# Optimization experiments

Hardware: AMD Instinct MI355X
Metric: run time of the kernel (lower is better)

The kernel has to match this reference:

```python
import jax, jax.numpy as jnp
import numpy as np
from math import comb

N_DERIV = 4          # num_derivatives
ODE_DIM = 512        # ode_dimension
K = ODE_DIM * (N_DERIV + 1)


def _build_system(n, d):
    # system_matrices_1d: A_1d = flip(pascal), Q_1d = flip(hilbert), chol(Q_1d)
    x = np.arange(n + 1)
    B = np.array([[comb(i, j) for j in range(n + 1)] for i in range(n + 1)], dtype=np.float64)
    A1 = B[::-1, ::-1]                                  # flip both axes
    Hil = 1.0 / (x[:, None] + x[None, :] + 1.0)
    Q1 = Hil[::-1, ::-1]
    L1 = np.linalg.cholesky(Q1)
    a = np.kron(np.eye(d), A1)
    q = np.kron(np.eye(d), L1)
    return jnp.asarray(a, jnp.float32), jnp.asarray(q, jnp.float32)


def _qr_r(x):
    # sqrtm_to_cholesky: upper-triangular factor from reduced QR
    return jnp.linalg.qr(x)[1]


def setup_inputs() -> dict:
    key = jax.random.key(0)
    k1, k2, k3, k4, k5 = jax.random.split(key, 5)
    a, q_sqrtm_lower = _build_system(N_DERIV, ODE_DIM)
    m0 = jax.random.normal(k1, (K,), dtype=jnp.float32)
    l0 = jnp.tril(jax.random.normal(k2, (K, K), dtype=jnp.float32) * 0.05)
    H = jax.random.normal(k3, (ODE_DIM, K), dtype=jnp.float32) * 0.1
    bias = jax.random.normal(k4, (ODE_DIM,), dtype=jnp.float32)
    dt = jax.random.uniform(k5, (1,), dtype=jnp.float32, minval=0.05, maxval=0.15)
    return {"m0": m0, "l0": l0, "H": H, "bias": bias, "dt": dt,
            "a": a, "q_sqrtm_lower": q_sqrtm_lower}


def reference(m0, l0, H, bias, dt, a, q_sqrtm_lower):
    d = H.shape[0]
    k = m0.shape[0]
    n1 = k // d                       # num_derivatives + 1
    # --- assemble_preconditioner ---
    powers = jnp.arange(n1 - 1, -1, -1, dtype=m0.dtype)
    scales = jnp.exp(jax.lax.lgamma(powers + 1.0))
    pw = powers + 0.5
    adt = jnp.abs(dt[0])
    p = jnp.tile(adt ** pw / scales, d)          # (k,)
    p_inv = jnp.tile(adt ** (-pw) * scales, d)   # (k,)
    # --- extrapolate_mean ---
    m0_p = p_inv * m0
    m_ext_p = a @ m0_p
    m_ext = p * m_ext_p
    # EK-style linearized observation residual
    m_obs = H @ m_ext - bias                     # (d,)
    # --- estimate_error ---
    l_obs_ns_e = H @ (p_inv[:, None] * q_sqrtm_lower)            # (d,k)
    l_obs_raw = _qr_r(l_obs_ns_e.T).T                            # lower (d,d)
    res_white = jax.scipy.linalg.solve_triangular(l_obs_raw.T, m_obs, lower=False)
    diffusion = jnp.sqrt(jnp.dot(res_white, res_white) / res_white.size)
    error = diffusion * jnp.sqrt(jnp.einsum('nj,nj->n', l_obs_raw, l_obs_raw))
    # --- complete_extrapolation (sum_of_sqrtm_factors) ---
    R1 = (a @ (p_inv[:, None] * l0)).T           # (k,k)
    R2 = (diffusion * q_sqrtm_lower).T           # (k,k)
    l_ext_p = _qr_r(jnp.vstack([R1, R2])).T      # lower (k,k)
    l_ext = p[:, None] * l_ext_p
    # --- final_correction ---
    l_obs_ns = H @ l_ext                         # (d,k)
    l_obs = _qr_r(l_obs_ns.T).T                  # lower (d,d)
    crosscov = l_ext @ l_obs_ns.T                # (k,d)
    gain = jax.scipy.linalg.cho_solve((l_obs, True), crosscov.T).T  # (k,d)
    m_cor = m_ext - gain @ m_obs
    l_cor = l_ext - gain @ l_obs_ns
    u = jnp.reshape(m_cor, (-1, d), order='F')[0]  # derivative-0 block
    return m_cor, l_cor, u, error, diffusion
```

## Files before the change

### kernel.cpp

```cpp
#include <hip/hip_runtime.h>
#include <math.h>

#define KDIM 2560
#define DDIM 512
#define NB 64

#define QM 2560
#define QM2 1024
#define QN 512
#define PW 32
#define UW 3
#define QACT 544

#define OUT_LCOR 2560
#define OUT_U    6556160
#define OUT_ERR  6556672
#define OUT_DIFF 6557184


__global__ void k_setup(const float* dt, double* scal){
  if (threadIdx.x==0 && blockIdx.x==0){
    double adt = fabs((double)dt[0]);
    const double scales[5] = {24.0,6.0,2.0,1.0,1.0};
    for (int i=0;i<5;i++){
      double pw = (double)(4-i)+0.5;
      scal[i]   = pow(adt, pw)/scales[i];
      scal[5+i] = pow(adt,-pw)*scales[i];
    }
  }
}

__global__ __launch_bounds__(256) void k_mext_mobs(const float* a, const float* m0, const float* H,
                                                   const float* bias, const double* scal,
                                                   double* mext, double* mobs){
  __shared__ double me[KDIM];
  __shared__ double red[256];
  double pp[5], pv[5];
  #pragma unroll
  for (int i=0;i<5;i++){ pp[i]=scal[i]; pv[i]=scal[5+i]; }
  int tid=threadIdx.x;
  for (int r=tid; r<KDIM; r+=256){
    int j=r/5, i=r%5;
    const float* arow = a + (size_t)r*KDIM + 5*j;
    const float* m0b  = m0 + 5*j;
    double acc=0;
    #pragma unroll
    for (int l=0;l<5;l++) acc += (double)arow[l]*pv[l]*(double)m0b[l];
    me[r] = pp[i]*acc;
  }
  __syncthreads();
  if (blockIdx.x==0) for (int r=tid;r<KDIM;r+=256) mext[r]=me[r];
  int b = blockIdx.x;
  const float* Hr = H + (size_t)b*KDIM;
  double acc=0;
  for (int c=tid;c<KDIM;c+=256) acc += (double)Hr[c]*me[c];
  red[tid]=acc; __syncthreads();
  for (int s=128;s>0;s>>=1){ if (tid<s) red[tid]+=red[tid+s]; __syncthreads(); }
  if (tid==0) mobs[b] = red[0] - (double)bias[b];
}

__global__ void k_A2(const float* H, const float* q, const double* scal,
                     double* Atop, double* Abot){
  int idx = blockIdx.x*blockDim.x+threadIdx.x;
  if (idx >= QN*QM) return;
  double pv[5];
  #pragma unroll
  for (int t=0;t<5;t++) pv[t]=scal[5+t];
  int j = idx / QM;
  int i = idx % QM;
  int bi = i/5;
  double acc=0;
  #pragma unroll
  for (int t=0;t<5;t++)
    acc += (double)H[(size_t)j*QM + 5*bi+t]*pv[t]*(double)q[(size_t)(5*bi+t)*QM + i];
  if (i < 512) Atop[(size_t)j*QM2 + i] = acc;
  else         Abot[(size_t)j*2048 + (i-512)] = acc;
}

__global__ void k_copyB(const double* Gbot, double* AQ){
  int idx = blockIdx.x*blockDim.x+threadIdx.x;
  if (idx >= 512*512) return;
  int c = idx/512, rr = idx%512;
  AQ[(size_t)c*QM2 + 512 + rr] = (rr<=c) ? Gbot[(size_t)c*512 + rr] : 0.0;
}

__global__ __launch_bounds__(576) void qr_panel(double* A, double* vhead, int col0, double* Tbuf){
  __shared__ double redw[9][PW];
  __shared__ double rednorm[9];
  __shared__ double sh[3];
  __shared__ double wsh[PW];
  __shared__ double alphas[PW], betas[PW];
  __shared__ double VtVs[PW][PW];
  __shared__ double Tsh[PW][PW];
  int tid=threadIdx.x, wid=tid>>6, lane=tid&63;
  int m = QM2 - col0; if (m > QACT) m = QACT;
  bool on = tid < m;
  double x[PW];
  #pragma unroll
  for (int j=0;j<PW;j++)
    x[j] = on ? A[(size_t)(col0+j)*QM2 + col0 + tid] : 0.0;
  for (int j=0;j<PW;j++){
    double v0 = (tid>=j && on)? x[j] : 0.0;
    double ps = v0*v0;
    #pragma unroll
    for (int o=32;o>0;o>>=1) ps += __shfl_down(ps,o);
    if (lane==0) rednorm[wid]=ps;
    if (tid==j) sh[0]=x[j];
    __syncthreads();
    if (tid==0){
      double s0=0;
      for (int t=0;t<9;t++) s0+=rednorm[t];
      double x1=sh[0];
      double nrm=sqrt(s0);
      double alpha=(x1>=0.0)?-nrm:nrm;
      double v1=x1-alpha;
      double vtv=s0-2.0*alpha*x1+alpha*alpha;
      double b=(vtv>0.0)?2.0/vtv:0.0;
      sh[1]=v1; sh[2]=b;
      alphas[j]=alpha; betas[j]=b;
      vhead[col0+j]=v1;
    }
    __syncthreads();
    if (tid==j) x[j]=sh[1];
    double b=sh[2];
    double v=(tid>=j && on)? x[j] : 0.0;
    #pragma unroll
    for (int t=0;t<PW;t++){
      if (t==j) continue;
      double p=v*x[t];
      #pragma unroll
      for (int o=32;o>0;o>>=1) p+=__shfl_down(p,o);
      if (lane==0) redw[wid][t]=p;
    }
    __syncthreads();
    if (tid<PW && tid!=j){
      double tot=0;
      #pragma unroll
      for (int t2=0;t2<9;t2++) tot+=redw[t2][tid];
      if (tid>j) wsh[tid]=b*tot;
      else       VtVs[tid][j]=tot;
    }
    __syncthreads();
    if (v!=0.0){
      for (int t=j+1;t<PW;t++) x[t]-=wsh[t]*v;
    }
  }
  __syncthreads();
  if (tid<PW){
    int i=tid;
    Tsh[i][i]=betas[i];
    for (int j2=i+1;j2<PW;j2++){
      double z=0;
      for (int t=i;t<j2;t++) z+=Tsh[i][t]*VtVs[t][j2];
      Tsh[i][j2]=-betas[j2]*z;
    }
  }
  __syncthreads();
  for (int e=tid;e<PW*PW;e+=576){
    int i=e/PW, j2=e%PW;
    Tbuf[e] = (j2>=i)? Tsh[i][j2] : 0.0;
  }
  if (on){
    #pragma unroll
    for (int j=0;j<PW;j++)
      A[(size_t)(col0+j)*QM2 + col0 + tid] = (tid==j)? alphas[j] : x[j];
  }
}

__global__ __launch_bounds__(256) void qr_update(double* A, const double* vhead,
                                                 const double* Tbuf, int col0){
  __shared__ double redu[4][PW];
  __shared__ double ysh[PW];
  __shared__ double wsh[PW];
  int tid=threadIdx.x, wid=tid>>6, lane=tid&63;
  int cc=col0+PW+blockIdx.x;
  int m=QM2-col0; if (m > QACT) m = QACT;
  double a[UW];
  #pragma unroll
  for (int w=0;w<UW;w++){
    int lr=tid+w*256;
    a[w]=(lr<m)? A[(size_t)cc*QM2+col0+lr] : 0.0;
  }
  double acc[PW];
  #pragma unroll
  for (int j=0;j<PW;j++) acc[j]=0;
  #pragma unroll
  for (int w=0;w<UW;w++){
    int lr=tid+w*256;
    if (lr<m){
      #pragma unroll
      for (int j=0;j<PW;j++){
        double vj;
        if (lr>j)       vj=A[(size_t)(col0+j)*QM2+col0+lr];
        else if (lr==j) vj=vhead[col0+j];
        else            vj=0.0;
        acc[j]+=vj*a[w];
      }
    }
  }
  #pragma unroll
  for (int j=0;j<PW;j++){
    double d=acc[j];
    #pragma unroll
    for (int o=32;o>0;o>>=1) d+=__shfl_down(d,o);
    if (lane==0) redu[wid][j]=d;
  }
  __syncthreads();
  if (tid<PW){
    double y=0;
    #pragma unroll
    for (int t=0;t<4;t++) y+=redu[t][tid];
    ysh[tid]=y;
  }
  __syncthreads();
  if (tid<PW){
    double s=0;
    for (int t=0;t<=tid;t++) s+=Tbuf[t*PW+tid]*ysh[t];
    wsh[tid]=s;
  }
  __syncthreads();
  #pragma unroll
  for (int w=0;w<UW;w++){
    int lr=tid+w*256;
    if (lr<m){
      double s=0;
      #pragma unroll
      for (int j=0;j<PW;j++){
        double vj;
        if (lr>j)       vj=A[(size_t)(col0+j)*QM2+col0+lr];
        else if (lr==j) vj=vhead[col0+j];
        else            vj=0.0;
        s+=vj*wsh[j];
      }
      A[(size_t)cc*QM2+col0+lr]=a[w]-s;
    }
  }
}

__global__ __launch_bounds__(512) void k_rpost(const double* Aq, const double* mobs,
                                               double* scal, float* out){
  __shared__ double b[DDIM];
  __shared__ double xs[DDIM];
  __shared__ double D[NB][NB+1];
  __shared__ double red[DDIM];
  __shared__ double g1sh[DDIM];
  int tid=threadIdx.x;
  {
    double s=0;
    for (int r=0;r<=tid;r++){ double v=Aq[(size_t)tid*QM2 + r]; s+=v*v; }
    g1sh[tid]=s;
  }
  b[tid]=mobs[tid];
  __syncthreads();
  for (int p=7;p>=0;p--){
    int b0=p*NB;
    for (int e=tid;e<NB*NB;e+=512){ int i=e&63, j2=e>>6; D[i][j2]=Aq[(size_t)(b0+j2)*QM2 + b0+i]; }
    __syncthreads();
    if (tid<64){
      double bi=b[b0+tid];
      for (int k=NB-1;k>=0;k--){
        double bk=__shfl(bi,k);
        double xk=bk/D[k][k];
        if (tid<k) bi-=D[tid][k]*xk;
        if (tid==k) bi=xk;
      }
      xs[b0+tid]=bi;
    }
    __syncthreads();
    if (tid<b0){
      double s=0;
      #pragma unroll 8
      for (int j2=0;j2<NB;j2++) s+=Aq[(size_t)(b0+j2)*QM2 + tid]*xs[b0+j2];
      b[tid]-=s;
    }
    __syncthreads();
  }
  red[tid]=xs[tid]*xs[tid]; __syncthreads();
  for (int s=256;s>0;s>>=1){ if (tid<s) red[tid]+=red[tid+s]; __syncthreads(); }
  double diff=sqrt(red[0]/(double)DDIM);
  if (tid==0){ scal[10]=diff; out[OUT_DIFF]=(float)diff; }
  out[OUT_ERR+tid]=(float)(diff*sqrt(fmax(g1sh[tid],0.0)));
}

__global__ void k_X(const float* a, const float* l0, const double* scal, float* X){
  int idx=blockIdx.x*blockDim.x+threadIdx.x;
  if (idx>=KDIM*KDIM) return;
  double pv[5];
  #pragma unroll
  for (int t=0;t<5;t++) pv[t]=scal[5+t];
  int r=idx/KDIM, c=idx%KDIM;
  int j=r/5;
  const float* arow = a + (size_t)r*KDIM + 5*j;
  double acc=0;
  #pragma unroll
  for (int l=0;l<5;l++)
    acc += (double)arow[l]*pv[l]*(double)l0[(size_t)(5*j+l)*KDIM+c];
  X[idx]=(float)acc;
}

template<typename TA,int ATR,typename TB,int BTR,int MODE>
__global__ __launch_bounds__(256) void gemm64(const TA* __restrict__ A,int lda,
                                              const TB* __restrict__ B,int ldb,
                                              void* __restrict__ Cv,int ldc,
                                              int K,int kmode){
  __shared__ double As[16][65];
  __shared__ double Bs[16][65];
  int tid=threadIdx.x, tx=tid&15, ty=tid>>4;
  int n0=blockIdx.x*64, m0=blockIdx.y*64;
  int ks=0, ke=K;
  if (kmode==1) ks=n0;
  else if (kmode==2) ke=min(K,n0+64);
  else if (kmode==3) ke=min(K,m0+64);
  else if (kmode==4) ks=m0;
  double acc[4][4]={};
  for (int k0=ks;k0<ke;k0+=16){
    if (ATR){
      for (int e=tid;e<16*64;e+=256){int k=e>>6,mm=e&63; As[k][mm]=(double)A[(size_t)(k0+k)*lda+m0+mm];}
    } else {
      for (int e=tid;e<64*16;e+=256){int mm=e>>4,k=e&15; As[k][mm]=(double)A[(size_t)(m0+mm)*lda+k0+k];}
    }
    if (BTR){
      for (int e=tid;e<64*16;e+=256){int nn=e>>4,k=e&15; Bs[k][nn]=(double)B[(size_t)(n0+nn)*ldb+k0+k];}
    } else {
      for (int e=tid;e<16*64;e+=256){int k=e>>6,nn=e&63; Bs[k][nn]=(double)B[(size_t)(k0+k)*ldb+n0+nn];}
    }
    __syncthreads();
    #pragma unroll
    for (int t=0;t<16;t++){
      double av[4],bv[4];
      #pragma unroll
      for (int i=0;i<4;i++){av[i]=As[t][ty+16*i];bv[i]=Bs[t][tx+16*i];}
      #pragma unroll
      for (int i=0;i<4;i++)
        #pragma unroll
        for (int j=0;j<4;j++) acc[i][j]+=av[i]*bv[j];
    }
    __syncthreads();
  }
  #pragma unroll
  for (int i=0;i<4;i++){
    #pragma unroll
    for (int j=0;j<4;j++){
      size_t idx=(size_t)(m0+ty+16*i)*ldc+n0+tx+16*j;
      if (MODE==0) ((double*)Cv)[idx]=acc[i][j];
      else if (MODE==1) ((double*)Cv)[idx]-=acc[i][j];
      else ((float*)Cv)[idx]=(float)acc[i][j];
    }
  }
}

__global__ __launch_bounds__(256) void syrk_lower(const float* __restrict__ X, const float* __restrict__ q,
                                                  const double* __restrict__ scal,
                                                  double* __restrict__ G, int n){
  int t = blockIdx.x;
  int u = (int)((sqrtf(8.0f*(float)t+1.0f)+1.0f)*0.5f);
  while ((u*(u-1))/2 > t) u--;
  while ((u*(u+1))/2 <= t) u++;
  int s = (KDIM/64) - u;
  int r = s + (t - (u*(u-1))/2);
  int S0=s*64, R0=r*64;
  __shared__ double As[16][65];
  __shared__ double Bs[16][65];
  int tid=threadIdx.x, tx=tid&15, ty=tid>>4;
  int kend=min(n, S0+80);
  double acc[4][4]={};
  for (int k0=0;k0<kend;k0+=16){
    for (int e=tid;e<64*16;e+=256){int mm=e>>4,k=e&15; As[k][mm]=(double)X[(size_t)(R0+mm)*n+k0+k];}
    for (int e=tid;e<64*16;e+=256){int nn=e>>4,k=e&15; Bs[k][nn]=(double)X[(size_t)(S0+nn)*n+k0+k];}
    __syncthreads();
    #pragma unroll
    for (int t2=0;t2<16;t2++){
      double av[4],bv[4];
      #pragma unroll
      for (int i=0;i<4;i++){av[i]=As[t2][ty+16*i];bv[i]=Bs[t2][tx+16*i];}
      #pragma unroll
      for (int i=0;i<4;i++)
        #pragma unroll
        for (int j=0;j<4;j++) acc[i][j]+=av[i]*bv[j];
    }
    __syncthreads();
  }
  double dd = scal[10]*scal[10];
  #pragma unroll
  for (int i=0;i<4;i++)
    #pragma unroll
    for (int j=0;j<4;j++){
      int rr=R0+ty+16*i, c=S0+tx+16*j;
      double v=acc[i][j];
      if (c<=rr && (rr/5)==(c/5)){
        double qq=0;
        #pragma unroll
        for (int k=0;k<5;k++) qq += (double)q[(size_t)(rr%5)*KDIM+k]*(double)q[(size_t)(c%5)*KDIM+k];
        v += dd*qq;
      }
      G[(size_t)rr*n+c]=v;
    }
}

__global__ __launch_bounds__(256) void chol_diag(double* A, int n, int k0){
  __shared__ double P[NB][NB+1];
  int tid=threadIdx.x;
  for (int e=tid;e<NB*NB;e+=256){int r=e>>6,c=e&63;P[r][c]=A[(size_t)(k0+r)*n+k0+c];}
  int tx=tid&15, ty=tid>>4;
  __syncthreads();
  for (int j=0;j<NB;j++){
    double pj=P[j][j];
    __syncthreads();
    double rpj=1.0/sqrt(fmax(pj,1e-280));
    if (tid>j && tid<NB) P[tid][j]*=rpj;
    if (tid==j) P[j][j]=sqrt(fmax(pj,1e-280));
    __syncthreads();
    #pragma unroll
    for (int a2=0;a2<4;a2++){
      int r=ty+16*a2;
      double lrj=P[r][j];
      #pragma unroll
      for (int b2=0;b2<4;b2++){
        int c=tx+16*b2;
        if (r>j && c>j && c<=r) P[r][c]-=lrj*P[c][j];
      }
    }
    __syncthreads();
  }
  for (int e=tid;e<NB*NB;e+=256){int r=e>>6,c=e&63;A[(size_t)(k0+r)*n+k0+c]=P[r][c];}
}

__global__ __launch_bounds__(256) void chol_trsm(double* A,int n,int k0){
  __shared__ double Ls[NB][NB+1];
  __shared__ double St[NB][NB+1];
  __shared__ double rec[NB];
  int tid=threadIdx.x;
  for (int e=tid;e<NB*NB;e+=256){int r=e>>6,c=e&63;Ls[r][c]=A[(size_t)(k0+r)*n+k0+c];}
  __syncthreads();
  if (tid<NB) rec[tid]=1.0/Ls[tid][tid];
  int base=k0+NB+blockIdx.x*256;
  int myrow=base+tid;
  int mychunk=tid>>6, lrow=tid&63;
  double ar[NB];
  for (int ch=0;ch<4;ch++){
    int r0=base+ch*64;
    for (int e=tid;e<NB*NB;e+=256){
      int r=e>>6,c=e&63;
      if (r0+r<n) St[r][c]=A[(size_t)(r0+r)*n+k0+c];
    }
    __syncthreads();
    if (mychunk==ch && myrow<n){
      #pragma unroll
      for (int c=0;c<NB;c++) ar[c]=St[lrow][c];
    }
    __syncthreads();
  }
  if (myrow<n){
    #pragma unroll
    for (int j=0;j<NB;j++){
      double s=ar[j];
      #pragma unroll
      for (int t=0;t<j;t++) s-=ar[t]*Ls[j][t];
      ar[j]=s*rec[j];
    }
  }
  for (int ch=0;ch<4;ch++){
    int r0=base+ch*64;
    if (mychunk==ch && myrow<n){
      #pragma unroll
      for (int c=0;c<NB;c++) St[lrow][c]=ar[c];
    }
    __syncthreads();
    for (int e=tid;e<NB*NB;e+=256){
      int r=e>>6,c=e&63;
      if (r0+r<n) A[(size_t)(r0+r)*n+k0+c]=St[r][c];
    }
    __syncthreads();
  }
}

__global__ __launch_bounds__(256) void chol_syrk_fd(double* A,int n,int k0){
  int ts0=k0+NB;
  int t=blockIdx.x;
  int r=(int)((sqrtf(8.0f*(float)t+1.0f)-1.0f)*0.5f);
  while ((r*(r+1))/2 > t) r--;
  while (((r+1)*(r+2))/2 <= t) r++;
  int s=t-(r*(r+1))/2;
  int S0=ts0+s*64, R0=ts0+r*64;
  __shared__ double As[16][65];
  __shared__ double Bs[16][65];
  __shared__ double P[NB][NB+1];
  int tid=threadIdx.x, tx=tid&15, ty=tid>>4;
  double acc[4][4]={};
  for (int k0i=0;k0i<NB;k0i+=16){
    for (int e=tid;e<64*16;e+=256){int mm=e>>4,k=e&15; As[k][mm]=A[(size_t)(R0+mm)*n+k0+k0i+k];}
    for (int e=tid;e<64*16;e+=256){int nn=e>>4,k=e&15; Bs[k][nn]=A[(size_t)(S0+nn)*n+k0+k0i+k];}
    __syncthreads();
    #pragma unroll
    for (int tt=0;tt<16;tt++){
      double av[4],bv[4];
      #pragma unroll
      for (int i=0;i<4;i++){av[i]=As[tt][ty+16*i];bv[i]=Bs[tt][tx+16*i];}
      #pragma unroll
      for (int i=0;i<4;i++)
        #pragma unroll
        for (int j=0;j<4;j++) acc[i][j]+=av[i]*bv[j];
    }
    __syncthreads();
  }
  if (t!=0){
    #pragma unroll
    for (int i=0;i<4;i++)
      #pragma unroll
      for (int j=0;j<4;j++)
        A[(size_t)(R0+ty+16*i)*n+S0+tx+16*j]-=acc[i][j];
    return;
  }
  #pragma unroll
  for (int i=0;i<4;i++)
    #pragma unroll
    for (int j=0;j<4;j++)
      P[ty+16*i][tx+16*j] = A[(size_t)(R0+ty+16*i)*n+S0+tx+16*j] - acc[i][j];
  __syncthreads();
  for (int j=0;j<NB;j++){
    double pj=P[j][j];
    __syncthreads();
    double rpj=1.0/sqrt(fmax(pj,1e-280));
    if (tid>j && tid<NB) P[tid][j]*=rpj;
    if (tid==j) P[j][j]=sqrt(fmax(pj,1e-280));
    __syncthreads();
    #pragma unroll
    for (int a2=0;a2<4;a2++){
      int r2=ty+16*a2;
      double lrj=P[r2][j];
      #pragma unroll
      for (int b2=0;b2<4;b2++){
        int c=tx+16*b2;
        if (r2>j && c>j && c<=r2) P[r2][c]-=lrj*P[c][j];
      }
    }
    __syncthreads();
  }
  for (int e=tid;e<NB*NB;e+=256){int r2=e>>6,c=e&63;A[(size_t)(ts0+r2)*n+ts0+c]=P[r2][c];}
}

__global__ void k_extract(const double* G2, const double* scal, float* lext){
  int idx=blockIdx.x*blockDim.x+threadIdx.x;
  if (idx>=KDIM*KDIM) return;
  int r=idx/KDIM, c=idx%KDIM;
  double v = (c<=r)? scal[r%5]*G2[idx] : 0.0;
  lext[idx]=(float)v;
}

__global__ __launch_bounds__(256) void trinv_diag(const double* S, double* Linv){
  __shared__ double Ls[NB][NB+1];
  __shared__ double Ti[NB][NB+1];
  int jb=blockIdx.x, tid=threadIdx.x;
  for (int e=tid; e<DDIM*NB; e+=256){
    int r=e/NB, c=e%NB;
    Linv[(size_t)r*DDIM + jb*NB + c]=0.0;
  }
  for (int e=tid;e<NB*NB;e+=256){int r=e>>6,c=e&63; Ls[r][c]=S[(size_t)(jb*NB+r)*DDIM + jb*NB+c];}
  __syncthreads();
  if (tid<NB){
    int c=tid;
    for (int r=c;r<NB;r++){
      double s=(r==c)?1.0:0.0;
      for (int t=c;t<r;t++) s-=Ls[r][t]*Ti[t][c];
      Ti[r][c]=s/Ls[r][r];
    }
    for (int r=0;r<c;r++) Ti[r][c]=0.0;
  }
  __syncthreads();
  for (int e=tid;e<NB*NB;e+=256){int r=e>>6,c=e&63; Linv[(size_t)(jb*NB+r)*DDIM + jb*NB+c]=Ti[r][c];}
}

__global__ __launch_bounds__(256) void trinv_step(const double* S, double* Linv, int d){
  __shared__ double As[16][65];
  __shared__ double Bs[16][65];
  __shared__ double Ps[NB][NB+1];
  int jb=blockIdx.x, ib=jb+d;
  int tid=threadIdx.x, tx=tid&15, ty=tid>>4;
  double acc[4][4]={};
  int kstart=jb*NB, kend=ib*NB;
  for (int k0=kstart;k0<kend;k0+=16){
    for (int e=tid;e<64*16;e+=256){int mm=e>>4,k=e&15; As[k][mm]=S[(size_t)(ib*NB+mm)*DDIM + k0+k];}
    for (int e=tid;e<16*64;e+=256){int k=e>>6,nn=e&63; Bs[k][nn]=Linv[(size_t)(k0+k)*DDIM + jb*NB+nn];}
    __syncthreads();
    #pragma unroll
    for (int t=0;t<16;t++){
      double av[4],bv[4];
      #pragma unroll
      for (int i=0;i<4;i++){av[i]=As[t][ty+16*i];bv[i]=Bs[t][tx+16*i];}
      #pragma unroll
      for (int i=0;i<4;i++)
        #pragma unroll
        for (int j=0;j<4;j++) acc[i][j]+=av[i]*bv[j];
    }
    __syncthreads();
  }
  #pragma unroll
  for (int i=0;i<4;i++)
    #pragma unroll
    for (int j=0;j<4;j++) Ps[ty+16*i][tx+16*j]=acc[i][j];
  double o[4][4]={};
  __syncthreads();
  for (int k0=0;k0<NB;k0+=16){
    for (int e=tid;e<64*16;e+=256){int mm=e>>4,k=e&15; As[k][mm]=Linv[(size_t)(ib*NB+mm)*DDIM + ib*NB+k0+k];}
    __syncthreads();
    #pragma unroll
    for (int t=0;t<16;t++){
      double av[4],bv[4];
      #pragma unroll
      for (int i=0;i<4;i++){av[i]=As[t][ty+16*i];bv[i]=Ps[k0+t][tx+16*i];}
      #pragma unroll
      for (int i=0;i<4;i++)
        #pragma unroll
        for (int j=0;j<4;j++) o[i][j]+=av[i]*bv[j];
    }
    __syncthreads();
  }
  #pragma unroll
  for (int i=0;i<4;i++)
    #pragma unroll
    for (int j=0;j<4;j++)
      Linv[(size_t)(ib*NB+ty+16*i)*DDIM + jb*NB+tx+16*j] = -o[i][j];
}

__global__ void k_mcor(const double* Z, const double* mobs, const double* mext, float* out){
  __shared__ double mo[DDIM];
  for (int s=threadIdx.x;s<DDIM;s+=256) mo[s]=mobs[s];
  __syncthreads();
  int r=blockIdx.x*256+threadIdx.x;
  if (r>=KDIM) return;
  double acc=0;
  for (int s=0;s<DDIM;s++) acc += Z[(size_t)s*KDIM+r]*mo[s];
  double mc = mext[r]-acc;
  out[r]=(float)mc;
  if (r%5==0) out[OUT_U + r/5]=(float)mc;
}

__global__ __launch_bounds__(256) void k_lcor(const double* __restrict__ Z, const float* __restrict__ lobs,
                                              const float* __restrict__ lext, float* __restrict__ out){
  __shared__ double As[16][65];
  __shared__ double Bs[16][65];
  int tid=threadIdx.x, tx=tid&15, ty=tid>>4;
  int n0=blockIdx.x*64, m0=blockIdx.y*64;
  double acc[4][4]={};
  for (int k0=0;k0<DDIM;k0+=16){
    for (int e=tid;e<16*64;e+=256){int k=e>>6,mm=e&63; As[k][mm]=Z[(size_t)(k0+k)*KDIM+m0+mm];}
    for (int e=tid;e<16*64;e+=256){int k=e>>6,nn=e&63; Bs[k][nn]=(double)lobs[(size_t)(k0+k)*KDIM+n0+nn];}
    __syncthreads();
    #pragma unroll
    for (int t=0;t<16;t++){
      double av[4],bv[4];
      #pragma unroll
      for (int i=0;i<4;i++){av[i]=As[t][ty+16*i];bv[i]=Bs[t][tx+16*i];}
      #pragma unroll
      for (int i=0;i<4;i++)
        #pragma unroll
        for (int j=0;j<4;j++) acc[i][j]+=av[i]*bv[j];
    }
    __syncthreads();
  }
  #pragma unroll
  for (int i=0;i<4;i++)
    #pragma unroll
    for (int j=0;j<4;j++){
      size_t idx=(size_t)(m0+ty+16*i)*KDIM+n0+tx+16*j;
      out[OUT_LCOR+idx]=(float)((double)lext[idx]-acc[i][j]);
    }
}

extern "C" void kernel_launch(void* const* d_in, const int* in_sizes, int n_in,
                              void* d_out, int out_size, void* d_ws, size_t ws_size,
                              hipStream_t stream) {
  const float* m0  = (const float*)d_in[0];
  const float* l0  = (const float*)d_in[1];
  const float* H   = (const float*)d_in[2];
  const float* bias= (const float*)d_in[3];
  const float* dt  = (const float*)d_in[4];
  const float* a   = (const float*)d_in[5];
  const float* q   = (const float*)d_in[6];
  float* out = (float*)d_out;

  char* w=(char*)d_ws;
  auto alloc=[&](size_t bytes)->char*{ char* p=w; w += ((bytes+255)/256)*256; return p; };
  double* scal  =(double*)alloc(16*8);
  double* mext  =(double*)alloc((size_t)KDIM*8);
  double* mobs  =(double*)alloc((size_t)DDIM*8);
  double* vheadA=(double*)alloc((size_t)QN*8);
  double* Tbuf  =(double*)alloc((size_t)PW*PW*8);
  double* AQ    =(double*)alloc((size_t)QM2*QN*8);
  double* S     =(double*)alloc((size_t)DDIM*DDIM*8);
  double* G2    =(double*)alloc((size_t)KDIM*KDIM*8);
  float*  LOBS  =(float*) alloc((size_t)DDIM*KDIM*4);
  float*  X     =(float*) alloc((size_t)KDIM*KDIM*4);
  float*  LEXT  = X;
  double* Abot  = G2;
  double* Gbot  = Abot + (size_t)2048*512;
  double* Linv  = G2;
  double* C2    = Linv + (size_t)DDIM*DDIM;
  double* Y     = C2   + (size_t)DDIM*KDIM;
  double* Z     = Y    + (size_t)DDIM*KDIM;

  auto chol_full=[&](double* M, int n){
    chol_diag<<<1,256,0,stream>>>(M, n, 0);
    for (int k0=0;k0+NB<n;k0+=NB){
      int m = n-k0-NB;
      chol_trsm<<<(m+255)/256,256,0,stream>>>(M,n,k0);
      int T = m/64;
      chol_syrk_fd<<<T*(T+1)/2,256,0,stream>>>(M,n,k0);
    }
  };

  k_setup<<<1,1,0,stream>>>(dt, scal);
  k_mext_mobs<<<DDIM,256,0,stream>>>(a, m0, H, bias, scal, mext, mobs);

  k_A2<<<(QN*QM+255)/256,256,0,stream>>>(H, q, scal, AQ, Abot);
  gemm64<double,0,double,1,0><<<dim3(8,8),256,0,stream>>>(Abot,2048, Abot,2048, Gbot,512, 2048, 0);
  chol_full(Gbot, 512);
  k_copyB<<<(512*512+255)/256,256,0,stream>>>(Gbot, AQ);
  for (int p=0;p<QN/PW;p++){
    int col0=p*PW;
    qr_panel<<<1,576,0,stream>>>(AQ, vheadA, col0, Tbuf);
    int ntr = QN - col0 - PW;
    if (ntr>0) qr_update<<<ntr,256,0,stream>>>(AQ, vheadA, Tbuf, col0);
  }
  k_rpost<<<1,512,0,stream>>>(AQ, mobs, scal, out);

  k_X<<<(KDIM*KDIM+255)/256,256,0,stream>>>(a, l0, scal, X);
  syrk_lower<<<(KDIM/64)*((KDIM/64)+1)/2,256,0,stream>>>(X, q, scal, G2, KDIM);
  chol_full(G2, KDIM);
  k_extract<<<(KDIM*KDIM+255)/256,256,0,stream>>>(G2, scal, LEXT);

  gemm64<float,0,float,0,2><<<dim3(KDIM/64,DDIM/64),256,0,stream>>>(H,KDIM, LEXT,KDIM, LOBS,KDIM, KDIM, 1);
  gemm64<float,0,float,1,0><<<dim3(DDIM/64,DDIM/64),256,0,stream>>>(LOBS,KDIM, LOBS,KDIM, S,DDIM, KDIM, 0);
  chol_full(S, DDIM);
  trinv_diag<<<8,256,0,stream>>>(S, Linv);
  for (int d=1;d<8;d++)
    trinv_step<<<8-d,256,0,stream>>>(S, Linv, d);
  gemm64<float,0,float,1,0><<<dim3(KDIM/64,DDIM/64),256,0,stream>>>(LOBS,KDIM, LEXT,KDIM, C2,KDIM, KDIM, 2);
  gemm64<double,0,double,0,0><<<dim3(KDIM/64,DDIM/64),256,0,stream>>>(Linv,DDIM, C2,KDIM, Y,KDIM, DDIM, 3);
  gemm64<double,1,double,0,0><<<dim3(KDIM/64,DDIM/64),256,0,stream>>>(Linv,DDIM, Y,KDIM, Z,KDIM, DDIM, 4);

  k_mcor<<<(KDIM+255)/256,256,0,stream>>>(Z, mobs, mext, out);
  k_lcor<<<dim3(KDIM/64,KDIM/64),256,0,stream>>>(Z, LOBS, LEXT, out);
}
```

Before: 18.24 ms.

## Add single-block Cholesky for small trailing blocks and narrow QR panel width

Result: faster. 16.74 ms (-8.2%).

```diff
diff --git a/kernel.cpp b/kernel.cpp
--- a/kernel.cpp
+++ b/kernel.cpp
@@ -8,9 +8,9 @@
 #define QM 2560
 #define QM2 1024
 #define QN 512
-#define PW 32
+#define PW 16
 #define UW 3
-#define QACT 544
+#define QACT 528
 
 #define OUT_LCOR 2560
 #define OUT_U    6556160
@@ -99,6 +99,7 @@
   #pragma unroll
   for (int j=0;j<PW;j++)
     x[j] = on ? A[(size_t)(col0+j)*QM2 + col0 + tid] : 0.0;
+  #pragma unroll
   for (int j=0;j<PW;j++){
     double v0 = (tid>=j && on)? x[j] : 0.0;
     double ps = v0*v0;
@@ -142,6 +143,7 @@
     }
     __syncthreads();
     if (v!=0.0){
+      #pragma unroll
       for (int t=j+1;t<PW;t++) x[t]-=wsh[t]*v;
     }
   }
@@ -474,7 +476,7 @@
   }
 }
 
-__global__ __launch_bounds__(256) void chol_syrk_fd(double* A,int n,int k0){
+__global__ __launch_bounds__(256) void chol_syrk_fd(double* A,int n,int k0,int fuse){
   int ts0=k0+NB;
   int t=blockIdx.x;
   int r=(int)((sqrtf(8.0f*(float)t+1.0f)-1.0f)*0.5f);
@@ -503,7 +505,7 @@
     }
     __syncthreads();
   }
-  if (t!=0){
+  if (t!=0 || !fuse){
     #pragma unroll
     for (int i=0;i<4;i++)
       #pragma unroll
@@ -537,6 +539,114 @@
     __syncthreads();
   }
   for (int e=tid;e<NB*NB;e+=256){int r2=e>>6,c=e&63;A[(size_t)(ts0+r2)*n+ts0+c]=P[r2][c];}
+}
+
+__global__ __launch_bounds__(256) void chol_block(double* A, int ld, int n){
+  __shared__ double pool[64*65 + 64 + 32*65];
+  double (*Ls)[NB+1] = (double(*)[NB+1])pool;
+  double* rec        = pool + 64*65;
+  double (*St)[NB+1] = (double(*)[NB+1])(pool + 64*65 + 64);
+  double (*As)[65]   = (double(*)[65])(pool + 64*65 + 64);
+  double (*Bs)[65]   = (double(*)[65])(pool + 64*65 + 64 + 16*65);
+  int tid=threadIdx.x, tx=tid&15, ty=tid>>4;
+  for (int k0=0;k0<n;k0+=NB){
+    for (int e=tid;e<NB*NB;e+=256){int r=e>>6,c=e&63;Ls[r][c]=A[(size_t)(k0+r)*ld+k0+c];}
+    __syncthreads();
+    for (int j=0;j<NB;j++){
+      double pj=Ls[j][j];
+      __syncthreads();
+      double rpj=1.0/sqrt(fmax(pj,1e-280));
+      if (tid>j && tid<NB) Ls[tid][j]*=rpj;
+      if (tid==j) Ls[j][j]=sqrt(fmax(pj,1e-280));
+      __syncthreads();
+      #pragma unroll
+      for (int a2=0;a2<4;a2++){
+        int r=ty+16*a2;
+        double lrj=Ls[r][j];
+        #pragma unroll
+        for (int b2=0;b2<4;b2++){
+          int c=tx+16*b2;
+          if (r>j && c>j && c<=r) Ls[r][c]-=lrj*Ls[c][j];
+        }
+      }
+      __syncthreads();
+    }
+    for (int e=tid;e<NB*NB;e+=256){int r=e>>6,c=e&63;A[(size_t)(k0+r)*ld+k0+c]=Ls[r][c];}
+    if (tid<NB) rec[tid]=1.0/Ls[tid][tid];
+    __syncthreads();
+    int m=n-k0-NB;
+    if (m<=0) break;
+    for (int base=k0+NB;base<n;base+=256){
+      int myrow=base+tid, mychunk=tid>>5, lrow=tid&31;
+      double ar[NB];
+      for (int ch=0;ch<8;ch++){
+        int r0=base+ch*32;
+        for (int e=tid;e<32*NB;e+=256){
+          int r=e>>6,c=e&63;
+          if (r0+r<n) St[r][c]=A[(size_t)(r0+r)*ld+k0+c];
+        }
+        __syncthreads();
+        if (mychunk==ch && myrow<n){
+          #pragma unroll
+          for (int c=0;c<NB;c++) ar[c]=St[lrow][c];
+        }
+        __syncthreads();
+      }
+      if (myrow<n){
+        #pragma unroll
+        for (int j=0;j<NB;j++){
+          double s=ar[j];
+          #pragma unroll
+          for (int t=0;t<j;t++) s-=ar[t]*Ls[j][t];
+          ar[j]=s*rec[j];
+        }
+      }
+      for (int ch=0;ch<8;ch++){
+        int r0=base+ch*32;
+        if (mychunk==ch && myrow<n){
+          #pragma unroll
+          for (int c=0;c<NB;c++) St[lrow][c]=ar[c];
+        }
+        __syncthreads();
+        for (int e=tid;e<32*NB;e+=256){
+          int r=e>>6,c=e&63;
+          if (r0+r<n) A[(size_t)(r0+r)*ld+k0+c]=St[r][c];
+        }
+        __syncthreads();
+      }
+    }
+    int T=m/NB, ntile=T*(T+1)/2;
+    for (int t=0;t<ntile;t++){
+      int r=(int)((sqrtf(8.0f*(float)t+1.0f)-1.0f)*0.5f);
+      while ((r*(r+1))/2 > t) r--;
+      while (((r+1)*(r+2))/2 <= t) r++;
+      int s=t-(r*(r+1))/2;
+      int R0=k0+NB+r*NB, S0=k0+NB+s*NB;
+      double acc[4][4]={};
+      for (int k0i=0;k0i<NB;k0i+=16){
+        for (int e=tid;e<64*16;e+=256){int mm=e>>4,k=e&15; As[k][mm]=A[(size_t)(R0+mm)*ld+k0+k0i+k];}
+        for (int e=tid;e<64*16;e+=256){int nn=e>>4,k=e&15; Bs[k][nn]=A[(size_t)(S0+nn)*ld+k0+k0i+k];}
+        __syncthreads();
+        #pragma unroll
+        for (int tt=0;tt<16;tt++){
+          double av[4],bv[4];
+          #pragma unroll
+          for (int i=0;i<4;i++){av[i]=As[tt][ty+16*i];bv[i]=Bs[tt][tx+16*i];}
+          #pragma unroll
+          for (int i=0;i<4;i++)
+            #pragma unroll
+            for (int j=0;j<4;j++) acc[i][j]+=av[i]*bv[j];
+        }
+        __syncthreads();
+      }
+      #pragma unroll
+      for (int i=0;i<4;i++)
+        #pragma unroll
+        for (int j=0;j<4;j++)
+          A[(size_t)(R0+ty+16*i)*ld+S0+tx+16*j]-=acc[i][j];
+    }
+    __syncthreads();
+  }
 }
 
 __global__ void k_extract(const double* G2, const double* scal, float* lext){
@@ -700,12 +810,18 @@
   double* Z     = Y    + (size_t)DDIM*KDIM;
 
   auto chol_full=[&](double* M, int n){
+    if (n<=512){ chol_block<<<1,256,0,stream>>>(M, n, n); return; }
     chol_diag<<<1,256,0,stream>>>(M, n, 0);
     for (int k0=0;k0+NB<n;k0+=NB){
       int m = n-k0-NB;
       chol_trsm<<<(m+255)/256,256,0,stream>>>(M,n,k0);
       int T = m/64;
-      chol_syrk_fd<<<T*(T+1)/2,256,0,stream>>>(M,n,k0);
+      if (m<=512){
+        chol_syrk_fd<<<T*(T+1)/2,256,0,stream>>>(M,n,k0,0);
+        chol_block<<<1,256,0,stream>>>(M + (size_t)(k0+NB)*n + (k0+NB), n, m);
+        break;
+      }
+      chol_syrk_fd<<<T*(T+1)/2,256,0,stream>>>(M,n,k0,1);
     }
   };
 
```
